# Kernel optimization log

Hardware: AMD Instinct MI355X
Metric: run time of the kernel (lower is better)

## Reference

```python
import jax, jax.numpy as jnp
import numpy as np

H_DIM = 1024
N_HEADS = 16
SEQ_LEN = 2048
BATCH = 4


def setup_inputs() -> dict:
    key = jax.random.key(0)
    ks = jax.random.split(key, 9)
    s = 1.0 / np.sqrt(H_DIM)
    return {
        "x": jax.random.normal(ks[0], (BATCH, SEQ_LEN, H_DIM), dtype=jnp.float32),
        "Wq": jax.random.normal(ks[1], (H_DIM, H_DIM), dtype=jnp.float32) * s,
        "bq": jax.random.normal(ks[2], (H_DIM,), dtype=jnp.float32) * 0.01,
        "Wk": jax.random.normal(ks[3], (H_DIM, H_DIM), dtype=jnp.float32) * s,
        "bk": jax.random.normal(ks[4], (H_DIM,), dtype=jnp.float32) * 0.01,
        "Wv": jax.random.normal(ks[5], (H_DIM, H_DIM), dtype=jnp.float32) * s,
        "bv": jax.random.normal(ks[6], (H_DIM,), dtype=jnp.float32) * 0.01,
        "Wo": jax.random.normal(ks[7], (H_DIM, H_DIM), dtype=jnp.float32) * s,
        "bo": jax.random.normal(ks[8], (H_DIM,), dtype=jnp.float32) * 0.01,
    }


def reference(x, Wq, bq, Wk, bk, Wv, bv, Wo, bo):
    B, T, C = x.shape
    N = N_HEADS
    D = C // N
    # projections -> [B, N, T, D]
    def split_heads(t):
        return t.reshape(B, T, N, D).transpose(0, 2, 1, 3)
    q = split_heads(x @ Wq + bq)
    k = split_heads(x @ Wk + bk)
    v = split_heads(x @ Wv + bv)
    scale = 1.0 / jnp.sqrt(jnp.asarray(D, dtype=x.dtype))
    logits = jnp.einsum("bntd,bnsd->bnts", q, k) * scale  # [B,N,T,T]
    causal = jnp.tril(jnp.ones((T, T), dtype=bool))
    logits = jnp.where(causal[None, None], logits, jnp.asarray(-jnp.inf, dtype=x.dtype))
    attn = jax.nn.softmax(logits, axis=-1)
    ctx = jnp.einsum("bnts,bnsd->bntd", attn, v)  # [B,N,T,D]
    ctx = ctx.transpose(0, 2, 1, 3).reshape(B, T, C)
    return ctx @ Wo + bo
```

## Files before the change

kernel.cpp:

```cpp
#include <hip/hip_runtime.h>
#include <hip/hip_bf16.h>


typedef __attribute__((ext_vector_type(8))) short bhalf8;
typedef __attribute__((ext_vector_type(4))) float f32x4;

#define BATCH 4
#define SEQ 2048
#define CDIM 1024
#define NHEAD 16
#define HDIM 64
#define MTOT (BATCH * SEQ)
#define QSCALE 0.18033688011112042f

static __device__ inline unsigned short f2bf(float f) {
    unsigned int u = __float_as_uint(f);
    unsigned int r = (u + 0x7fffu + ((u >> 16) & 1u)) >> 16;
    return (unsigned short)r;
}
static __device__ inline float bf2f(unsigned short u) {
    return __uint_as_float(((unsigned int)u) << 16);
}
static __device__ inline f32x4 zero4() {
    f32x4 z = {0.f, 0.f, 0.f, 0.f};
    return z;
}
static __device__ inline f32x4 MFMA(bhalf8 a, bhalf8 b, f32x4 c) {
    return __builtin_amdgcn_mfma_f32_16x16x32_bf16(a, b, c, 0, 0, 0);
}
static __device__ inline void gload16(const void* g, void* l) {
    __builtin_amdgcn_global_load_lds(
        (const __attribute__((address_space(1))) unsigned int*)g,
        (__attribute__((address_space(3))) unsigned int*)l, 16, 0, 0);
}
static __device__ inline unsigned int pkbf16(float lo, float hi) {
    union { __hip_bfloat162 h; unsigned int u; } c;
    c.h = __float22bfloat162_rn(make_float2(lo, hi));
    return c.u;
}
static __device__ inline float exp2n(float x) {
    return __builtin_amdgcn_exp2f(x);
}

__global__ __launch_bounds__(256) void cast_x_kernel(const float* __restrict__ x,
                                                     short* __restrict__ o, int n8) {
    int i = blockIdx.x * 256 + threadIdx.x;
    if (i >= n8) return;
    const float4* xv = (const float4*)x;
    float4 a = xv[i * 2];
    float4 b = xv[i * 2 + 1];
    bhalf8 r;
    r[0] = (short)f2bf(a.x); r[1] = (short)f2bf(a.y);
    r[2] = (short)f2bf(a.z); r[3] = (short)f2bf(a.w);
    r[4] = (short)f2bf(b.x); r[5] = (short)f2bf(b.y);
    r[6] = (short)f2bf(b.z); r[7] = (short)f2bf(b.w);
    *(bhalf8*)(o + (size_t)i * 8) = r;
}

__global__ __launch_bounds__(256) void wtrans_kernel(const float* __restrict__ W0,
                                                     const float* __restrict__ W1,
                                                     const float* __restrict__ W2,
                                                     const float* __restrict__ W3,
                                                     short* __restrict__ out) {
    __shared__ float t[32][33];
    const float* W = (blockIdx.z == 0) ? W0 : (blockIdx.z == 1) ? W1
                     : (blockIdx.z == 2) ? W2 : W3;
    short* o = out + (size_t)blockIdx.z * CDIM * CDIM;
    int n0 = blockIdx.x * 32, k0 = blockIdx.y * 32;
    int tx = threadIdx.x, ty = threadIdx.y;
    for (int j = 0; j < 4; ++j)
        t[ty + j * 8][tx] = W[(size_t)(k0 + ty + j * 8) * CDIM + n0 + tx];
    __syncthreads();
    for (int j = 0; j < 4; ++j)
        o[(size_t)(n0 + ty + j * 8) * CDIM + k0 + tx] = (short)f2bf(t[tx][ty + j * 8]);
}

template <int MODE, int GN>
__global__ __launch_bounds__(256) void gemm128(const short* __restrict__ A,
                                               const short* __restrict__ Bt,
                                               const float* __restrict__ b0,
                                               const float* __restrict__ b1,
                                               const float* __restrict__ b2,
                                               unsigned short* __restrict__ QKout,
                                               unsigned short* __restrict__ Vout,
                                               float* __restrict__ Fout) {
    __shared__ char lds[32768];
    char* AlB0 = lds;
    char* BlB0 = lds + 16384;

    const int tid = threadIdx.x, lane = tid & 63, w = tid >> 6;
    const int g = lane >> 4, t16 = lane & 15;
    const int wr = w >> 1, wc = w & 1;

    const int f = blockIdx.x;
    const int xcd = f & 7, i = f >> 3;
    const int mt = xcd * 8 + i / GN, nt = i % GN;
    const int tm = mt * 128, tn = nt * 128;
    const int part = tn >> 10;
    const int tnp = tn & 1023;

    const int c0 = tid, c1 = 256 + tid;
    const int r0 = c0 >> 2, r1 = c1 >> 2;
    const int k0c = (c0 & 3) ^ ((r0 >> 1) & 3);
    const int k1c = (c1 & 3) ^ ((r1 >> 1) & 3);
    const short* a0 = A + (size_t)(tm + r0) * 1024 + k0c * 8;
    const short* a1 = A + (size_t)(tm + r1) * 1024 + k1c * 8;
    const short* bp0 = Bt + (size_t)(tn + r0) * 1024 + k0c * 8;
    const short* bp1 = Bt + (size_t)(tn + r1) * 1024 + k1c * 8;

    int aoff[4], boff[4];
#pragma unroll
    for (int mi = 0; mi < 4; ++mi) {
        int row = wr * 64 + mi * 16 + t16;
        aoff[mi] = row * 64 + ((g ^ ((row >> 1) & 3)) << 4);
    }
#pragma unroll
    for (int ni = 0; ni < 4; ++ni) {
        int row = wc * 64 + ni * 16 + t16;
        boff[ni] = row * 64 + ((g ^ ((row >> 1) & 3)) << 4);
    }

    f32x4 acc[4][4];
#pragma unroll
    for (int mi = 0; mi < 4; ++mi)
#pragma unroll
        for (int ni = 0; ni < 4; ++ni) acc[mi][ni] = zero4();

#define STAGE(kt_, bb_)                                                   \
    do {                                                                  \
        int off_ = (kt_) * 32;                                            \
        char* al_ = AlB0 + (bb_) * 8192;                                  \
        char* bl_ = BlB0 + (bb_) * 8192;                                  \
        gload16(a0 + off_, al_ + tid * 16);                               \
        gload16(a1 + off_, al_ + 4096 + tid * 16);                        \
        gload16(bp0 + off_, bl_ + tid * 16);                              \
        gload16(bp1 + off_, bl_ + 4096 + tid * 16);                       \
    } while (0)

    STAGE(0, 0);
    __syncthreads();

#pragma unroll 2
    for (int kt = 0; kt < 32; ++kt) {
        const int buf = kt & 1;
        if (kt + 1 < 32) STAGE(kt + 1, buf ^ 1);
        const char* al = AlB0 + buf * 8192;
        const char* bl = BlB0 + buf * 8192;
        bhalf8 af[4], bfr[4];
#pragma unroll
        for (int mi = 0; mi < 4; ++mi) af[mi] = *(const bhalf8*)(al + aoff[mi]);
#pragma unroll
        for (int ni = 0; ni < 4; ++ni) bfr[ni] = *(const bhalf8*)(bl + boff[ni]);
        __builtin_amdgcn_s_setprio(1);
#pragma unroll
        for (int mi = 0; mi < 4; ++mi)
#pragma unroll
            for (int ni = 0; ni < 4; ++ni)
                acc[mi][ni] = MFMA(af[mi], bfr[ni], acc[mi][ni]);
        __builtin_amdgcn_s_setprio(0);
        __syncthreads();
    }
#undef STAGE

    if (MODE == 0 && part == 2) {
#pragma unroll
        for (int mi = 0; mi < 4; ++mi)
#pragma unroll
            for (int ni = 0; ni < 4; ++ni) {
                int col_l = wc * 64 + ni * 16 + t16;
                float bias = b2[tnp + col_l];
#pragma unroll
                for (int r = 0; r < 4; ++r) {
                    int row_l = wr * 64 + mi * 16 + g * 4 + r;
                    int byte = col_l * 256 + ((row_l * 2) ^ ((col_l & 7) << 4));
                    *(unsigned short*)(lds + byte) = f2bf(acc[mi][ni][r] + bias);
                }
            }
        __syncthreads();
#pragma unroll
        for (int p = 0; p < 8; ++p) {
            int lin = p * 4096 + tid * 16;
            int rv = lin >> 8;
            int inrow = lin & 255;
            int phys = rv * 256 + (inrow ^ ((rv & 7) << 4));
            bhalf8 val = *(const bhalf8*)(lds + phys);
            int n_g = tnp + rv;
            int hh = n_g >> 6, d = n_g & 63;
            int m = tm + (inrow >> 1);
            int bi = m >> 11, t0 = m & 2047;
            *(bhalf8*)(Vout + (((size_t)((bi * NHEAD + hh) * HDIM + d)) << 11) + t0) = val;
        }
    } else {
#pragma unroll
        for (int mi = 0; mi < 4; ++mi)
#pragma unroll
            for (int ni = 0; ni < 4; ++ni) {
                int col_l = wc * 64 + ni * 16 + t16;
                float bias = 0.f;
                if (MODE == 0) bias = (part == 0 ? b0 : b1)[tnp + col_l];
#pragma unroll
                for (int r = 0; r < 4; ++r) {
                    int row_l = wr * 64 + mi * 16 + g * 4 + r;
                    float v = acc[mi][ni][r] + bias;
                    if (MODE == 0 && part == 0) v *= QSCALE;
                    int byte = row_l * 256 + ((col_l * 2) ^ (((row_l >> 2) & 3) << 5));
                    *(unsigned short*)(lds + byte) = f2bf(v);
                }
            }
        __syncthreads();
#pragma unroll
        for (int p = 0; p < 8; ++p) {
            int lin = p * 4096 + tid * 16;
            int row_l = lin >> 8;
            int inrow = lin & 255;
            int phys = row_l * 256 + ((inrow & ~31) ^ (((row_l >> 2) & 3) << 5)) + (inrow & 31);
            bhalf8 val = *(const bhalf8*)(lds + phys);
            int col0 = inrow >> 1;
            int m = tm + row_l;
            if (MODE == 1) {
                int n_g = tn + col0;
                float* op = Fout + (size_t)m * 1024 + n_g;
                float4 o0, o1;
                o0.x = bf2f((unsigned short)val[0]) + b0[n_g + 0];
                o0.y = bf2f((unsigned short)val[1]) + b0[n_g + 1];
                o0.z = bf2f((unsigned short)val[2]) + b0[n_g + 2];
                o0.w = bf2f((unsigned short)val[3]) + b0[n_g + 3];
                o1.x = bf2f((unsigned short)val[4]) + b0[n_g + 4];
                o1.y = bf2f((unsigned short)val[5]) + b0[n_g + 5];
                o1.z = bf2f((unsigned short)val[6]) + b0[n_g + 6];
                o1.w = bf2f((unsigned short)val[7]) + b0[n_g + 7];
                *(float4*)(op) = o0;
                *(float4*)(op + 4) = o1;
            } else {
                int n_g = tnp + col0;
                int bi = m >> 11, t = m & 2047;
                int hh = n_g >> 6, d0 = n_g & 63;
                *(bhalf8*)(QKout +
                           (((size_t)((part * 64 + bi * NHEAD + hh) * SEQ + t)) << 6) + d0) = val;
            }
        }
    }
}

__global__ __launch_bounds__(256) void attn_kernel(const short* __restrict__ Q,
                                                   const short* __restrict__ K,
                                                   const short* __restrict__ V,
                                                   unsigned short* __restrict__ ctx) {
    __shared__ short Kl[2][64 * 64];
    __shared__ short Vl[2][64 * 64];
    __shared__ short Pl[4][16 * 64];

    const int tid = threadIdx.x, lane = tid & 63, w = tid >> 6;
    const int g = lane >> 4, t16 = lane & 15;

    int orig = blockIdx.x;
    int swz = (orig & 7) * 128 + (orig >> 3);
    const int bh = swz >> 4;
    const int sp = swz & 15;

    const short* Qh = Q + ((size_t)bh << 17);
    const short* Kh = K + ((size_t)bh << 17);
    const short* Vh = V + ((size_t)bh << 17);

    int koff[2], voff[2], ldst[2];
#pragma unroll
    for (int it = 0; it < 2; ++it) {
        int c = it * 256 + tid;
        int srow = c >> 3;
        int dc = (c & 7) ^ (srow & 7);
        koff[it] = (srow << 6) + dc * 8;
        voff[it] = (srow << 11) + dc * 8;
        ldst[it] = it * 4096 + w * 1024;
    }

#define STAGE(kv_, bb_)                                                       \
    do {                                                                      \
        gload16(Kh + koff[0] + ((kv_) << 12), (char*)Kl[bb_] + ldst[0]);      \
        gload16(Kh + koff[1] + ((kv_) << 12), (char*)Kl[bb_] + ldst[1]);      \
        gload16(Vh + voff[0] + ((kv_) << 6), (char*)Vl[bb_] + ldst[0]);       \
        gload16(Vh + voff[1] + ((kv_) << 6), (char*)Vl[bb_] + ldst[1]);       \
    } while (0)

    const int b = bh >> 4, hh = bh & 15;
    const int swb = (t16 & 7) << 4;

    int buf = 0;
    STAGE(0, 0);

    for (int ph = 0; ph < 2; ++ph) {
        const int qti = (ph == 0) ? (31 - sp) : sp;
        const int qbase = qti * 64;
        const int ntile = qti + 1;

        bhalf8 qf0, qf1;
        {
            const short* qp = Qh + ((size_t)(qbase + w * 16 + t16) << 6) + g * 8;
            qf0 = *(const bhalf8*)(qp);
            qf1 = *(const bhalf8*)(qp + 32);
        }

        f32x4 acc[4];
#pragma unroll
        for (int i = 0; i < 4; ++i) acc[i] = zero4();
        float l = 0.f;

        __syncthreads();

        for (int kv = 0; kv < ntile; ++kv) {
            if (kv + 1 < ntile) STAGE(kv + 1, buf ^ 1);

            f32x4 lg[4];
            __builtin_amdgcn_s_setprio(1);
#pragma unroll
            for (int cb = 0; cb < 4; ++cb) {
                int s = cb * 16 + t16;
                int sw = (s & 7) << 4;
                const char* rowp = (const char*)Kl[buf] + s * 128;
                bhalf8 k0 = *(const bhalf8*)(rowp + ((g * 16) ^ sw));
                bhalf8 k1 = *(const bhalf8*)(rowp + ((64 + g * 16) ^ sw));
                f32x4 z = zero4();
                z = MFMA(k0, qf0, z);
                z = MFMA(k1, qf1, z);
                lg[cb] = z;
            }
            __builtin_amdgcn_s_setprio(0);

            if (kv == qti) {
                int rowl = w * 16 + t16;
#pragma unroll
                for (int cb = 0; cb < 4; ++cb) {
                    int key0 = cb * 16 + g * 4;
#pragma unroll
                    for (int r = 0; r < 4; ++r)
                        if (key0 + r > rowl) lg[cb][r] = -1e30f;
                }
            }

            {
                float s_ = 0.f;
                int rowbyte = t16 * 128;
#pragma unroll
                for (int cb = 0; cb < 4; ++cb) {
                    float e0 = exp2n(lg[cb][0]);
                    float e1 = exp2n(lg[cb][1]);
                    float e2 = exp2n(lg[cb][2]);
                    float e3 = exp2n(lg[cb][3]);
                    s_ += (e0 + e1) + (e2 + e3);
                    uint2 wv;
                    wv.x = pkbf16(e0, e1);
                    wv.y = pkbf16(e2, e3);
                    int byte = (rowbyte + cb * 32 + g * 8) ^ swb;
                    *(uint2*)((char*)Pl[w] + byte) = wv;
                }
                l += s_;
            }

            __builtin_amdgcn_s_setprio(1);
#pragma unroll
            for (int kk = 0; kk < 2; ++kk) {
                bhalf8 vf[4];
#pragma unroll
                for (int db = 0; db < 4; ++db) {
                    int d = db * 16 + t16;
                    int vbyte = d * 128 + ((kk * 64 + g * 16) ^ ((d & 7) << 4));
                    vf[db] = *(const bhalf8*)((const char*)Vl[buf] + vbyte);
                }
                int abyte = (t16 * 128 + kk * 64 + g * 16) ^ swb;
                bhalf8 pa = *(const bhalf8*)((const char*)Pl[w] + abyte);
#pragma unroll
                for (int db = 0; db < 4; ++db)
                    acc[db] = MFMA(pa, vf[db], acc[db]);
            }
            __builtin_amdgcn_s_setprio(0);

            __syncthreads();
            buf ^= 1;
        }

        if (ph == 0) STAGE(0, buf);

        float lt = l;
        lt += __shfl_xor(lt, 16, 64);
        lt += __shfl_xor(lt, 32, 64);
        float linv = 1.f / lt;
#pragma unroll
        for (int r = 0; r < 4; ++r) {
            float inv = __shfl(linv, g * 4 + r, 64);
            int t = qbase + w * 16 + g * 4 + r;
            size_t rowoff = (((size_t)(b * SEQ + t)) << 10) + hh * 64;
#pragma unroll
            for (int db = 0; db < 4; ++db)
                ctx[rowoff + db * 16 + t16] = f2bf(acc[db][r] * inv);
        }
    }
#undef STAGE
}

extern "C" void kernel_launch(void* const* d_in, const int* in_sizes, int n_in,
                              void* d_out, int out_size, void* d_ws, size_t ws_size,
                              hipStream_t stream) {
    const float* x  = (const float*)d_in[0];
    const float* Wq = (const float*)d_in[1];
    const float* bq = (const float*)d_in[2];
    const float* Wk = (const float*)d_in[3];
    const float* bk = (const float*)d_in[4];
    const float* Wv = (const float*)d_in[5];
    const float* bv = (const float*)d_in[6];
    const float* Wo = (const float*)d_in[7];
    const float* bo = (const float*)d_in[8];

    char* ws = (char*)d_ws;
    short* x16 = (short*)(ws);
    short* Wt  = (short*)(ws + (size_t)16 * 1024 * 1024);
    short* Wot = Wt + (size_t)3 * CDIM * CDIM;
    short* Qb  = (short*)(ws + (size_t)24 * 1024 * 1024);
    short* Vb  = (short*)(ws + (size_t)56 * 1024 * 1024);
    short* Ctx = (short*)(ws + (size_t)72 * 1024 * 1024);

    cast_x_kernel<<<dim3(MTOT * CDIM / 8 / 256), dim3(256), 0, stream>>>(
        x, x16, MTOT * CDIM / 8);
    wtrans_kernel<<<dim3(32, 32, 4), dim3(32, 8), 0, stream>>>(Wq, Wk, Wv, Wo, Wt);

    gemm128<0, 24><<<dim3(1536), dim3(256), 0, stream>>>(
        x16, Wt, bq, bk, bv, (unsigned short*)Qb, (unsigned short*)Vb, nullptr);

    attn_kernel<<<dim3(1024), dim3(256), 0, stream>>>(
        Qb, Qb + (size_t)64 * SEQ * HDIM, Vb, (unsigned short*)Ctx);

    gemm128<1, 8><<<dim3(512), dim3(256), 0, stream>>>(
        Ctx, Wot, bo, nullptr, nullptr, nullptr, nullptr, (float*)d_out);
}
```

Measured before the change: 182.2 us.

## Load V tiles directly into registers with double-buffered prefetch across phases

The attention kernel no longer stages V through LDS. Each lane now loads its V fragments straight from global memory into a register double buffer (va/vb), one tile ahead. The K prefetch index runs continuously across both causal phases, so the next phase's first tile is fetched during the previous phase's last iteration. This removes V LDS traffic and the LDS footprint, but adds register pressure and uncoalesced strided global reads of V (transposed layout, 2048-element stride).

```diff
diff --git a/kernel.cpp b/kernel.cpp
--- a/kernel.cpp
+++ b/kernel.cpp
@@ -33,13 +33,13 @@
         (const __attribute__((address_space(1))) unsigned int*)g,
         (__attribute__((address_space(3))) unsigned int*)l, 16, 0, 0);
 }
+static __device__ inline float exp2n(float x) {
+    return __builtin_amdgcn_exp2f(x);
+}
 static __device__ inline unsigned int pkbf16(float lo, float hi) {
     union { __hip_bfloat162 h; unsigned int u; } c;
     c.h = __float22bfloat162_rn(make_float2(lo, hi));
     return c.u;
-}
-static __device__ inline float exp2n(float x) {
-    return __builtin_amdgcn_exp2f(x);
 }
 
 __global__ __launch_bounds__(256) void cast_x_kernel(const float* __restrict__ x,
@@ -247,7 +247,6 @@
                                                    const short* __restrict__ V,
                                                    unsigned short* __restrict__ ctx) {
     __shared__ short Kl[2][64 * 64];
-    __shared__ short Vl[2][64 * 64];
     __shared__ short Pl[4][16 * 64];
 
     const int tid = threadIdx.x, lane = tid & 63, w = tid >> 6;
@@ -262,30 +261,94 @@
     const short* Kh = K + ((size_t)bh << 17);
     const short* Vh = V + ((size_t)bh << 17);
 
-    int koff[2], voff[2], ldst[2];
+    int koff[2], ldst[2];
 #pragma unroll
     for (int it = 0; it < 2; ++it) {
         int c = it * 256 + tid;
         int srow = c >> 3;
         int dc = (c & 7) ^ (srow & 7);
         koff[it] = (srow << 6) + dc * 8;
-        voff[it] = (srow << 11) + dc * 8;
         ldst[it] = it * 4096 + w * 1024;
     }
-
-#define STAGE(kv_, bb_)                                                       \
+    int vel[4];
+#pragma unroll
+    for (int db = 0; db < 4; ++db) vel[db] = (db * 16 + t16) * 2048 + g * 8;
+
+    const int b = bh >> 4, hh = bh & 15;
+    const int swb = (t16 & 7) << 4;
+    char* Pw = (char*)Pl[w];
+    const int n0 = 32 - sp;
+
+#define STAGEK(kv_, bb_)                                                      \
     do {                                                                      \
         gload16(Kh + koff[0] + ((kv_) << 12), (char*)Kl[bb_] + ldst[0]);      \
         gload16(Kh + koff[1] + ((kv_) << 12), (char*)Kl[bb_] + ldst[1]);      \
-        gload16(Vh + voff[0] + ((kv_) << 6), (char*)Vl[bb_] + ldst[0]);       \
-        gload16(Vh + voff[1] + ((kv_) << 6), (char*)Vl[bb_] + ldst[1]);       \
     } while (0)
 
-    const int b = bh >> 4, hh = bh & 15;
-    const int swb = (t16 & 7) << 4;
-
-    int buf = 0;
-    STAGE(0, 0);
+#define LOADV(VT, kv_)                                                        \
+    do {                                                                      \
+        const short* vp_ = Vh + ((kv_) << 6);                                 \
+        _Pragma("unroll") for (int db = 0; db < 4; ++db) {                    \
+            VT[db * 2]     = *(const bhalf8*)(vp_ + vel[db]);                 \
+            VT[db * 2 + 1] = *(const bhalf8*)(vp_ + vel[db] + 32);            \
+        }                                                                     \
+    } while (0)
+
+#define TILE(VT)                                                              \
+    do {                                                                      \
+        f32x4 lg[4];                                                          \
+        __builtin_amdgcn_s_setprio(1);                                        \
+        _Pragma("unroll") for (int cb = 0; cb < 4; ++cb) {                    \
+            int s_ = cb * 16 + t16;                                           \
+            int sw_ = (s_ & 7) << 4;                                          \
+            const char* rowp = (const char*)Kl[buf] + s_ * 128;               \
+            bhalf8 k0 = *(const bhalf8*)(rowp + ((g * 16) ^ sw_));            \
+            bhalf8 k1 = *(const bhalf8*)(rowp + ((64 + g * 16) ^ sw_));       \
+            f32x4 z = zero4();                                                \
+            z = MFMA(k0, qf0, z);                                             \
+            z = MFMA(k1, qf1, z);                                             \
+            lg[cb] = z;                                                       \
+        }                                                                     \
+        __builtin_amdgcn_s_setprio(0);                                        \
+        if (kv == qti) {                                                      \
+            int rowl = w * 16 + t16;                                          \
+            _Pragma("unroll") for (int cb = 0; cb < 4; ++cb) {                \
+                int key0 = cb * 16 + g * 4;                                   \
+                _Pragma("unroll") for (int r = 0; r < 4; ++r)                 \
+                    if (key0 + r > rowl) lg[cb][r] = -1e30f;                  \
+            }                                                                 \
+        }                                                                     \
+        {                                                                     \
+            float s_ = 0.f;                                                   \
+            int rowbyte = t16 * 128;                                          \
+            _Pragma("unroll") for (int cb = 0; cb < 4; ++cb) {                \
+                float e0 = exp2n(lg[cb][0]);                                  \
+                float e1 = exp2n(lg[cb][1]);                                  \
+                float e2 = exp2n(lg[cb][2]);                                  \
+                float e3 = exp2n(lg[cb][3]);                                  \
+                s_ += (e0 + e1) + (e2 + e3);                                  \
+                uint2 wv;                                                     \
+                wv.x = pkbf16(e0, e1);                                        \
+                wv.y = pkbf16(e2, e3);                                        \
+                int byte = (rowbyte + cb * 32 + g * 8) ^ swb;                 \
+                *(uint2*)(Pw + byte) = wv;                                    \
+            }                                                                 \
+            l += s_;                                                          \
+        }                                                                     \
+        __builtin_amdgcn_s_setprio(1);                                        \
+        _Pragma("unroll") for (int kk = 0; kk < 2; ++kk) {                    \
+            int abyte = (t16 * 128 + kk * 64 + g * 16) ^ swb;                 \
+            bhalf8 pa = *(const bhalf8*)(Pw + abyte);                         \
+            _Pragma("unroll") for (int db = 0; db < 4; ++db)                  \
+                acc[db] = MFMA(pa, VT[db * 2 + kk], acc[db]);                 \
+        }                                                                     \
+        __builtin_amdgcn_s_setprio(0);                                        \
+    } while (0)
+
+    bhalf8 va[8], vb[8];
+    STAGEK(0, 0);
+    LOADV(va, 0);
+    int j = 0;
 
     for (int ph = 0; ph < 2; ++ph) {
         const int qti = (ph == 0) ? (31 - sp) : sp;
@@ -306,78 +369,21 @@
 
         __syncthreads();
 
-        for (int kv = 0; kv < ntile; ++kv) {
-            if (kv + 1 < ntile) STAGE(kv + 1, buf ^ 1);
-
-            f32x4 lg[4];
-            __builtin_amdgcn_s_setprio(1);
-#pragma unroll
-            for (int cb = 0; cb < 4; ++cb) {
-                int s = cb * 16 + t16;
-                int sw = (s & 7) << 4;
-                const char* rowp = (const char*)Kl[buf] + s * 128;
-                bhalf8 k0 = *(const bhalf8*)(rowp + ((g * 16) ^ sw));
-                bhalf8 k1 = *(const bhalf8*)(rowp + ((64 + g * 16) ^ sw));
-                f32x4 z = zero4();
-                z = MFMA(k0, qf0, z);
-                z = MFMA(k1, qf1, z);
-                lg[cb] = z;
+        for (int kv = 0; kv < ntile; ++kv, ++j) {
+            const int buf = j & 1;
+            int jn = j + 1;
+            int kvn = (jn < n0) ? jn : jn - n0;
+            bool pre = jn < 33;
+            if (pre) STAGEK(kvn, buf ^ 1);
+            if (j & 1) {
+                if (pre) LOADV(va, kvn);
+                TILE(vb);
+            } else {
+                if (pre) LOADV(vb, kvn);
+                TILE(va);
             }
-            __builtin_amdgcn_s_setprio(0);
-
-            if (kv == qti) {
-                int rowl = w * 16 + t16;
-#pragma unroll
-                for (int cb = 0; cb < 4; ++cb) {
-                    int key0 = cb * 16 + g * 4;
-#pragma unroll
-                    for (int r = 0; r < 4; ++r)
-                        if (key0 + r > rowl) lg[cb][r] = -1e30f;
-                }
-            }
-
-            {
-                float s_ = 0.f;
-                int rowbyte = t16 * 128;
-#pragma unroll
-                for (int cb = 0; cb < 4; ++cb) {
-                    float e0 = exp2n(lg[cb][0]);
-                    float e1 = exp2n(lg[cb][1]);
-                    float e2 = exp2n(lg[cb][2]);
-                    float e3 = exp2n(lg[cb][3]);
-                    s_ += (e0 + e1) + (e2 + e3);
-                    uint2 wv;
-                    wv.x = pkbf16(e0, e1);
-                    wv.y = pkbf16(e2, e3);
-                    int byte = (rowbyte + cb * 32 + g * 8) ^ swb;
-                    *(uint2*)((char*)Pl[w] + byte) = wv;
-                }
-                l += s_;
-            }
-
-            __builtin_amdgcn_s_setprio(1);
-#pragma unroll
-            for (int kk = 0; kk < 2; ++kk) {
-                bhalf8 vf[4];
-#pragma unroll
-                for (int db = 0; db < 4; ++db) {
-                    int d = db * 16 + t16;
-                    int vbyte = d * 128 + ((kk * 64 + g * 16) ^ ((d & 7) << 4));
-                    vf[db] = *(const bhalf8*)((const char*)Vl[buf] + vbyte);
-                }
-                int abyte = (t16 * 128 + kk * 64 + g * 16) ^ swb;
-                bhalf8 pa = *(const bhalf8*)((const char*)Pl[w] + abyte);
-#pragma unroll
-                for (int db = 0; db < 4; ++db)
-                    acc[db] = MFMA(pa, vf[db], acc[db]);
-            }
-            __builtin_amdgcn_s_setprio(0);
-
             __syncthreads();
-            buf ^= 1;
         }
-
-        if (ph == 0) STAGE(0, buf);
 
         float lt = l;
         lt += __shfl_xor(lt, 16, 64);
@@ -393,7 +399,9 @@
                 ctx[rowoff + db * 16 + t16] = f2bf(acc[db][r] * inv);
         }
     }
-#undef STAGE
+#undef TILE
+#undef LOADV
+#undef STAGEK
 }
 
 extern "C" void kernel_launch(void* const* d_in, const int* in_sizes, int n_in,
```

New measurement: 242.0 us. 32.8% more time.
